# Performance work log

Hardware: AMD Instinct MI355X
Metric: run time of the kernel (lower is better)

## Reference

```python
import jax, jax.numpy as jnp
import numpy as np

S, B, K, H = 2048, 256, 64, 128  # seq_len, batch, process_dim, hidden_size


def softplus10(x):
    return jax.nn.softplus(10.0 * x) / 10.0


def setup_inputs() -> dict:
    key = jax.random.key(0)
    ks = jax.random.split(key, 10)
    sc = 0.1
    dt = jax.random.uniform(ks[0], (S, B), dtype=jnp.float32)
    seq_types = jax.random.randint(ks[1], (S, B), 0, K)  # in [0, K); K is padding idx
    h0 = jnp.zeros((B, H), dtype=jnp.float32)
    embed_W = jax.random.normal(ks[2], (K + 1, K), dtype=jnp.float32) * sc
    embed_W = embed_W.at[K].set(0.0)  # padding_idx row is zero
    W_ih = jax.random.normal(ks[3], (H, K), dtype=jnp.float32) * sc
    b_ih = jax.random.normal(ks[4], (H,), dtype=jnp.float32) * sc
    W_hh = jax.random.normal(ks[5], (H, H), dtype=jnp.float32) * sc
    b_hh = jax.random.normal(ks[6], (H,), dtype=jnp.float32) * sc
    dec_W = jax.random.normal(ks[7], (H, K + H), dtype=jnp.float32) * sc
    dec_b = jax.random.normal(ks[8], (H,), dtype=jnp.float32) * sc
    return {"dt": dt, "h0": h0, "embed_W": embed_W, "W_ih": W_ih, "b_ih": b_ih,
            "W_hh": W_hh, "b_hh": b_hh, "dec_W": dec_W, "dec_b": dec_b,
            "seq_types": seq_types}


def reference(dt, h0, embed_W, W_ih, b_ih, W_hh, b_hh, dec_W, dec_b, seq_types):
    # Per-event recurrence: h(t) = hidden_i * exp(-decay_i * dt_i)
    def step(h, inp):
        dt_t, ty_t = inp                     # [B], [B]
        x = embed_W[ty_t]                    # [B, K] embedding lookup
        concat = jnp.concatenate([x, h], axis=1)          # [B, K+H]
        decay = softplus10(concat @ dec_W.T + dec_b)      # [B, H]
        hidden = jnp.tanh(x @ W_ih.T + b_ih + h @ W_hh.T + b_hh)  # RNNCell tanh
        h_new = hidden * jnp.exp(-decay * dt_t[:, None])  # decayed hidden state
        return h_new, (hidden, decay, h_new)

    _, (hiddens, decays, hiddens_ti) = jax.lax.scan(step, h0, (dt, seq_types))
    # each: [S, B, H], matching the per-step lists of the torch module
    return hiddens, decays, hiddens_ti
```

## Files before the change

kernel.cpp:

```cpp
#include <hip/hip_runtime.h>

#define SEQ 2048
#define BAT 256
#define KD  64
#define HD  128
#define SBH 67108864u

typedef _Float16 half2v  __attribute__((ext_vector_type(2)));
typedef __fp16   fp16x2  __attribute__((ext_vector_type(2)));
typedef unsigned uint2v  __attribute__((ext_vector_type(2)));

template<int CTRL>
__device__ __forceinline__ float dpp_add(float keep, float send) {
    const int r = __builtin_amdgcn_update_dpp(0, __float_as_int(send),
                                              CTRL, 0xF, 0xF, true);
    return keep + __int_as_float(r);
}

__device__ __forceinline__ float xchg32(float v, int hi_half, int lane) {
#if __has_builtin(__builtin_amdgcn_permlane32_swap)
    uint2v r = __builtin_amdgcn_permlane32_swap(__float_as_uint(v),
                                                __float_as_uint(v),
                                                false, false);
    return __uint_as_float(hi_half ? r.x : r.y);
#else
    return __uint_as_float(__builtin_amdgcn_ds_bpermute(
        ((lane ^ 32) << 2), __float_as_uint(v)));
#endif
}

__device__ __forceinline__ int PK(float a, float b) {
    fp16x2 p = __builtin_amdgcn_cvt_pkrtz(a, b);
    return __builtin_bit_cast(int, p);
}

__device__ __forceinline__ float fdot2(int w, int h, float c) {
#if __has_builtin(__builtin_amdgcn_fdot2)
    return __builtin_amdgcn_fdot2(__builtin_bit_cast(half2v, w),
                                  __builtin_bit_cast(half2v, h), c, false);
#else
    half2v wv = __builtin_bit_cast(half2v, w), hv = __builtin_bit_cast(half2v, h);
    return fmaf((float)wv[1], (float)hv[1], fmaf((float)wv[0], (float)hv[0], c));
#endif
}

#define PIN(x) asm volatile("" : "+v"(x))
#define PIN4(v4) PIN(v4.x); PIN(v4.y); PIN(v4.z); PIN(v4.w)

#define STEP_BARRIER() do {                                   \
    asm volatile("s_waitcnt lgkmcnt(0)" ::: "memory");        \
    __builtin_amdgcn_s_barrier();                             \
    asm volatile("" ::: "memory");                            \
} while (0)

__global__ __launch_bounds__(128) void precompute_tables(
    const float* __restrict__ embed_W, const float* __restrict__ W_ih,
    const float* __restrict__ b_ih,    const float* __restrict__ b_hh,
    const float* __restrict__ dec_W,   const float* __restrict__ dec_b,
    float* __restrict__ tabH, float* __restrict__ tabD)
{
    __shared__ float x[KD];
    const int ty = blockIdx.x;
    const int r  = threadIdx.x;
    if (r < KD) x[r] = embed_W[ty * KD + r];
    __syncthreads();
    float ah = 0.f, ad = 0.f;
#pragma unroll
    for (int k = 0; k < KD; ++k) {
        const float xv = x[k];
        ah += xv * W_ih[r * KD + k];
        ad += xv * dec_W[r * (KD + HD) + k];
    }
    tabH[ty * HD + r] = ah + b_ih[r] + b_hh[r];
    tabD[ty * HD + r] = ad + dec_b[r];
}

__global__ __launch_bounds__(256, 1) void hawkes_rnn(
    const float* __restrict__ dt_g,  const float* __restrict__ h0,
    const float* __restrict__ W_hh,  const float* __restrict__ dec_W,
    const int*   __restrict__ seq_types,
    const float* __restrict__ tabH,  const float* __restrict__ tabD,
    float* __restrict__ out)
{
    __shared__ __align__(16) _Float16 h16[2][HD];
    __shared__ __align__(8) int2 dtty[SEQ + 2];
    __shared__ _Float16 tabLH[(KD + 1) * HD];
    __shared__ _Float16 tabLD[(KD + 1) * HD];

    const int b    = blockIdx.x;
    const int tid  = threadIdx.x;
    const int lane = tid & 63;
    const int b0 = lane & 1, b1 = (lane >> 1) & 1;
    const int b2 = (lane >> 2) & 1, b3 = (lane >> 3) & 1;
    const int b4 = (lane >> 4) & 1, b5 = (lane >> 5) & 1;
    const int G     = (tid >> 6) * 4 + b4 * 2 + b2;
    const int row   = 8 * G + 4 * b0 + 2 * b1 + b3;
    const int chunk = b0 | (b1 << 1) | (b3 << 2);

    for (int t = tid; t < SEQ; t += 256) {
        dtty[t] = make_int2(__float_as_int(dt_g[(size_t)t * BAT + b]),
                            seq_types[(size_t)t * BAT + b]);
    }
    if (tid < 2) dtty[SEQ + tid] = make_int2(0, 0);
    for (int i = tid; i < (KD + 1) * HD; i += 256) {
        tabLH[i] = (_Float16)tabH[i];
        tabLD[i] = (_Float16)tabD[i];
    }
    if (tid < HD) h16[0][tid] = (_Float16)h0[b * HD + tid];

    const size_t rstr = b5 ? (size_t)(KD + HD) : (size_t)HD;
    const float* wb = (b5 ? (dec_W + KD) : W_hh) + (size_t)(8 * G) * rstr
                      + chunk * 16;
#define LWROW(DA, DB, P) { \
    const float4 _a = *reinterpret_cast<const float4*>(P);        \
    const float4 _b = *reinterpret_cast<const float4*>((P) + 4);  \
    const float4 _c = *reinterpret_cast<const float4*>((P) + 8);  \
    const float4 _d = *reinterpret_cast<const float4*>((P) + 12); \
    DA = make_int4(PK(_a.x,_a.y), PK(_a.z,_a.w), PK(_b.x,_b.y), PK(_b.z,_b.w)); \
    DB = make_int4(PK(_c.x,_c.y), PK(_c.z,_c.w), PK(_d.x,_d.y), PK(_d.z,_d.w)); }
    int4 w0a,w0b,w1a,w1b,w2a,w2b,w3a,w3b,w4a,w4b,w5a,w5b,w6a,w6b,w7a,w7b;
    LWROW(w0a,w0b, wb + 0 * rstr)  LWROW(w1a,w1b, wb + 1 * rstr)
    LWROW(w2a,w2b, wb + 2 * rstr)  LWROW(w3a,w3b, wb + 3 * rstr)
    LWROW(w4a,w4b, wb + 4 * rstr)  LWROW(w5a,w5b, wb + 5 * rstr)
    LWROW(w6a,w6b, wb + 6 * rstr)  LWROW(w7a,w7b, wb + 7 * rstr)
#undef LWROW
    PIN4(w0a); PIN4(w0b); PIN4(w1a); PIN4(w1b);
    PIN4(w2a); PIN4(w2b); PIN4(w3a); PIN4(w3b);
    PIN4(w4a); PIN4(w4b); PIN4(w5a); PIN4(w5b);
    PIN4(w6a); PIN4(w6b); PIN4(w7a); PIN4(w7b);

    const _Float16* tabp = (b5 ? tabLD : tabLH) + row;

    unsigned off = (unsigned)(b * HD + row);

    __syncthreads();

    int2 pr_cur = dtty[0];
    int2 pr_nxt = dtty[1];
    float tab_cur = (float)tabp[pr_cur.y * HD];
    float tab_nxt = (float)tabp[pr_nxt.y * HD];

#define DOT16(A, WA, WB) \
    A = fdot2(WA.x, hv0.x, A); A = fdot2(WA.y, hv0.y, A); \
    A = fdot2(WA.z, hv0.z, A); A = fdot2(WA.w, hv0.w, A); \
    A = fdot2(WB.x, hv1.x, A); A = fdot2(WB.y, hv1.y, A); \
    A = fdot2(WB.z, hv1.z, A); A = fdot2(WB.w, hv1.w, A);

#define STEP(P, TT) { \
    const int2 pr_pf = dtty[(TT) + 2];                \
    const float tab_pf = (float)tabp[pr_pf.y * HD];   \
    const float dtv = __int_as_float(pr_cur.x); \
     \
    const int4 hv0 = *reinterpret_cast<const int4*>(&h16[P][chunk * 16]); \
    const int4 hv1 = *reinterpret_cast<const int4*>(&h16[P][chunk * 16 + 8]); \
    float a0 = 0.f, a1 = 0.f, a2 = 0.f, a3 = 0.f; \
    float a4 = 0.f, a5 = 0.f, a6 = 0.f, a7 = 0.f; \
    DOT16(a0, w0a, w0b)  DOT16(a1, w1a, w1b) \
    DOT16(a2, w2a, w2b)  DOT16(a3, w3a, w3b) \
    DOT16(a4, w4a, w4b)  DOT16(a5, w5a, w5b) \
    DOT16(a6, w6a, w6b)  DOT16(a7, w7a, w7b) \
     \
    const float t0 = dpp_add<0xB1>(b0 ? a4 : a0, b0 ? a0 : a4); \
    const float t1 = dpp_add<0xB1>(b0 ? a5 : a1, b0 ? a1 : a5); \
    const float t2 = dpp_add<0xB1>(b0 ? a6 : a2, b0 ? a2 : a6); \
    const float t3 = dpp_add<0xB1>(b0 ? a7 : a3, b0 ? a3 : a7); \
     \
    const float u0 = dpp_add<0x4E>(b1 ? t2 : t0, b1 ? t0 : t2); \
    const float u1 = dpp_add<0x4E>(b1 ? t3 : t1, b1 ? t1 : t3); \
     \
    const float sv = dpp_add<0x128>(b3 ? u1 : u0, b3 ? u0 : u1) + tab_cur; \
     \
    const float e2 = __expf(2.f * sv); \
    const float vh = 1.f - __fdividef(2.f, e2 + 1.f);             \
    const float z  = 10.f * sv; \
    const float em = __expf(-fabsf(z)); \
    const float sp = 0.1f * (fmaxf(z, 0.f) + __logf(1.f + em));   \
    const float vd = __expf(-sp * dtv); \
    const float v  = b5 ? vd : vh; \
     \
    const float cross = xchg32(v, b5, lane); \
    const float hnew  = v * cross; \
    if (b5 == 0) { \
        h16[(P) ^ 1][row] = (_Float16)hnew;    \
        out[off] = v; \
        out[off + 2u * SBH] = hnew; \
    } else { \
        out[off + SBH] = sp; \
    } \
    off += BAT * HD; \
    pr_cur = pr_nxt;   pr_nxt = pr_pf; \
    tab_cur = tab_nxt; tab_nxt = tab_pf; \
    STEP_BARRIER(); \
}

    for (int t = 0; t < SEQ; t += 2) {
        STEP(0, t)
        STEP(1, t + 1)
    }
#undef STEP
#undef DOT16
}

extern "C" void kernel_launch(void* const* d_in, const int* in_sizes, int n_in,
                              void* d_out, int out_size, void* d_ws, size_t ws_size,
                              hipStream_t stream) {
    const float* dt        = (const float*)d_in[0];
    const float* h0        = (const float*)d_in[1];
    const float* embed_W   = (const float*)d_in[2];
    const float* W_ih      = (const float*)d_in[3];
    const float* b_ih      = (const float*)d_in[4];
    const float* W_hh      = (const float*)d_in[5];
    const float* b_hh      = (const float*)d_in[6];
    const float* dec_W     = (const float*)d_in[7];
    const float* dec_b     = (const float*)d_in[8];
    const int*   seq_types = (const int*)  d_in[9];
    float* out  = (float*)d_out;

    float* tabHw = (float*)d_ws;
    float* tabDw = tabHw + (KD + 1) * HD;

    precompute_tables<<<KD + 1, 128, 0, stream>>>(embed_W, W_ih, b_ih, b_hh,
                                                  dec_W, dec_b, tabHw, tabDw);
    hawkes_rnn<<<BAT, 256, 0, stream>>>(dt, h0, W_hh, dec_W, seq_types,
                                        tabHw, tabDw, out);
}
```

Baseline: 824.4 us.

## Map one thread per hidden row computing both hidden and decay dot products

Reworks the recurrent kernel from 256 threads, where each lane computes a partial 16-element dot product for 8 rows, to 128 threads, where each thread owns one hidden row and computes both full 128-length dot products (W_hh and the dec_W hidden part). This removes the DPP reduction tree and the permlane32 cross-half exchange, and each thread now writes all three outputs. In exchange, each thread holds twice as many packed-fp16 weight registers (128 VGPRs of weights), reads the whole h vector from LDS each step, and runs a longer serial dot-product chain per step.

```diff
diff --git a/kernel.cpp b/kernel.cpp
--- a/kernel.cpp
+++ b/kernel.cpp
@@ -8,26 +8,6 @@
 
 typedef _Float16 half2v  __attribute__((ext_vector_type(2)));
 typedef __fp16   fp16x2  __attribute__((ext_vector_type(2)));
-typedef unsigned uint2v  __attribute__((ext_vector_type(2)));
-
-template<int CTRL>
-__device__ __forceinline__ float dpp_add(float keep, float send) {
-    const int r = __builtin_amdgcn_update_dpp(0, __float_as_int(send),
-                                              CTRL, 0xF, 0xF, true);
-    return keep + __int_as_float(r);
-}
-
-__device__ __forceinline__ float xchg32(float v, int hi_half, int lane) {
-#if __has_builtin(__builtin_amdgcn_permlane32_swap)
-    uint2v r = __builtin_amdgcn_permlane32_swap(__float_as_uint(v),
-                                                __float_as_uint(v),
-                                                false, false);
-    return __uint_as_float(hi_half ? r.x : r.y);
-#else
-    return __uint_as_float(__builtin_amdgcn_ds_bpermute(
-        ((lane ^ 32) << 2), __float_as_uint(v)));
-#endif
-}
 
 __device__ __forceinline__ int PK(float a, float b) {
     fp16x2 p = __builtin_amdgcn_cvt_pkrtz(a, b);
@@ -75,7 +55,7 @@
     tabD[ty * HD + r] = ad + dec_b[r];
 }
 
-__global__ __launch_bounds__(256, 1) void hawkes_rnn(
+__global__ __launch_bounds__(128, 1) void hawkes_rnn(
     const float* __restrict__ dt_g,  const float* __restrict__ h0,
     const float* __restrict__ W_hh,  const float* __restrict__ dec_W,
     const int*   __restrict__ seq_types,
@@ -87,49 +67,46 @@
     __shared__ _Float16 tabLH[(KD + 1) * HD];
     __shared__ _Float16 tabLD[(KD + 1) * HD];
 
-    const int b    = blockIdx.x;
-    const int tid  = threadIdx.x;
-    const int lane = tid & 63;
-    const int b0 = lane & 1, b1 = (lane >> 1) & 1;
-    const int b2 = (lane >> 2) & 1, b3 = (lane >> 3) & 1;
-    const int b4 = (lane >> 4) & 1, b5 = (lane >> 5) & 1;
-    const int G     = (tid >> 6) * 4 + b4 * 2 + b2;
-    const int row   = 8 * G + 4 * b0 + 2 * b1 + b3;
-    const int chunk = b0 | (b1 << 1) | (b3 << 2);
-
-    for (int t = tid; t < SEQ; t += 256) {
+    const int b   = blockIdx.x;
+    const int tid = threadIdx.x;
+    const int row = tid;
+
+    for (int t = tid; t < SEQ; t += 128) {
         dtty[t] = make_int2(__float_as_int(dt_g[(size_t)t * BAT + b]),
                             seq_types[(size_t)t * BAT + b]);
     }
     if (tid < 2) dtty[SEQ + tid] = make_int2(0, 0);
-    for (int i = tid; i < (KD + 1) * HD; i += 256) {
+    for (int i = tid; i < (KD + 1) * HD; i += 128) {
         tabLH[i] = (_Float16)tabH[i];
         tabLD[i] = (_Float16)tabD[i];
     }
-    if (tid < HD) h16[0][tid] = (_Float16)h0[b * HD + tid];
-
-    const size_t rstr = b5 ? (size_t)(KD + HD) : (size_t)HD;
-    const float* wb = (b5 ? (dec_W + KD) : W_hh) + (size_t)(8 * G) * rstr
-                      + chunk * 16;
-#define LWROW(DA, DB, P) { \
-    const float4 _a = *reinterpret_cast<const float4*>(P);        \
-    const float4 _b = *reinterpret_cast<const float4*>((P) + 4);  \
-    const float4 _c = *reinterpret_cast<const float4*>((P) + 8);  \
-    const float4 _d = *reinterpret_cast<const float4*>((P) + 12); \
-    DA = make_int4(PK(_a.x,_a.y), PK(_a.z,_a.w), PK(_b.x,_b.y), PK(_b.z,_b.w)); \
-    DB = make_int4(PK(_c.x,_c.y), PK(_c.z,_c.w), PK(_d.x,_d.y), PK(_d.z,_d.w)); }
-    int4 w0a,w0b,w1a,w1b,w2a,w2b,w3a,w3b,w4a,w4b,w5a,w5b,w6a,w6b,w7a,w7b;
-    LWROW(w0a,w0b, wb + 0 * rstr)  LWROW(w1a,w1b, wb + 1 * rstr)
-    LWROW(w2a,w2b, wb + 2 * rstr)  LWROW(w3a,w3b, wb + 3 * rstr)
-    LWROW(w4a,w4b, wb + 4 * rstr)  LWROW(w5a,w5b, wb + 5 * rstr)
-    LWROW(w6a,w6b, wb + 6 * rstr)  LWROW(w7a,w7b, wb + 7 * rstr)
-#undef LWROW
-    PIN4(w0a); PIN4(w0b); PIN4(w1a); PIN4(w1b);
-    PIN4(w2a); PIN4(w2b); PIN4(w3a); PIN4(w3b);
-    PIN4(w4a); PIN4(w4b); PIN4(w5a); PIN4(w5b);
-    PIN4(w6a); PIN4(w6b); PIN4(w7a); PIN4(w7b);
-
-    const _Float16* tabp = (b5 ? tabLD : tabLH) + row;
+    h16[0][tid] = (_Float16)h0[b * HD + tid];
+
+    const float* wh = W_hh  + (size_t)row * HD;
+    const float* wd = dec_W + (size_t)row * (KD + HD) + KD;
+#define LQ(D, P) { \
+    const float4 _a = *reinterpret_cast<const float4*>(P);       \
+    const float4 _b = *reinterpret_cast<const float4*>((P) + 4); \
+    D = make_int4(PK(_a.x,_a.y), PK(_a.z,_a.w), PK(_b.x,_b.y), PK(_b.z,_b.w)); }
+    int4 wh0,wh1,wh2,wh3,wh4,wh5,wh6,wh7,wh8,wh9,wh10,wh11,wh12,wh13,wh14,wh15;
+    int4 wd0,wd1,wd2,wd3,wd4,wd5,wd6,wd7,wd8,wd9,wd10,wd11,wd12,wd13,wd14,wd15;
+    LQ(wh0,  wh +   0) LQ(wh1,  wh +   8) LQ(wh2,  wh +  16) LQ(wh3,  wh +  24)
+    LQ(wh4,  wh +  32) LQ(wh5,  wh +  40) LQ(wh6,  wh +  48) LQ(wh7,  wh +  56)
+    LQ(wh8,  wh +  64) LQ(wh9,  wh +  72) LQ(wh10, wh +  80) LQ(wh11, wh +  88)
+    LQ(wh12, wh +  96) LQ(wh13, wh + 104) LQ(wh14, wh + 112) LQ(wh15, wh + 120)
+    LQ(wd0,  wd +   0) LQ(wd1,  wd +   8) LQ(wd2,  wd +  16) LQ(wd3,  wd +  24)
+    LQ(wd4,  wd +  32) LQ(wd5,  wd +  40) LQ(wd6,  wd +  48) LQ(wd7,  wd +  56)
+    LQ(wd8,  wd +  64) LQ(wd9,  wd +  72) LQ(wd10, wd +  80) LQ(wd11, wd +  88)
+    LQ(wd12, wd +  96) LQ(wd13, wd + 104) LQ(wd14, wd + 112) LQ(wd15, wd + 120)
+#undef LQ
+    PIN4(wh0); PIN4(wh1); PIN4(wh2); PIN4(wh3);
+    PIN4(wh4); PIN4(wh5); PIN4(wh6); PIN4(wh7);
+    PIN4(wh8); PIN4(wh9); PIN4(wh10);PIN4(wh11);
+    PIN4(wh12);PIN4(wh13);PIN4(wh14);PIN4(wh15);
+    PIN4(wd0); PIN4(wd1); PIN4(wd2); PIN4(wd3);
+    PIN4(wd4); PIN4(wd5); PIN4(wd6); PIN4(wd7);
+    PIN4(wd8); PIN4(wd9); PIN4(wd10);PIN4(wd11);
+    PIN4(wd12);PIN4(wd13);PIN4(wd14);PIN4(wd15);
 
     unsigned off = (unsigned)(b * HD + row);
 
@@ -137,59 +114,64 @@
 
     int2 pr_cur = dtty[0];
     int2 pr_nxt = dtty[1];
-    float tab_cur = (float)tabp[pr_cur.y * HD];
-    float tab_nxt = (float)tabp[pr_nxt.y * HD];
-
-#define DOT16(A, WA, WB) \
-    A = fdot2(WA.x, hv0.x, A); A = fdot2(WA.y, hv0.y, A); \
-    A = fdot2(WA.z, hv0.z, A); A = fdot2(WA.w, hv0.w, A); \
-    A = fdot2(WB.x, hv1.x, A); A = fdot2(WB.y, hv1.y, A); \
-    A = fdot2(WB.z, hv1.z, A); A = fdot2(WB.w, hv1.w, A);
+    float tabH_cur = (float)tabLH[pr_cur.y * HD + row];
+    float tabD_cur = (float)tabLD[pr_cur.y * HD + row];
+    float tabH_nxt = (float)tabLH[pr_nxt.y * HD + row];
+    float tabD_nxt = (float)tabLD[pr_nxt.y * HD + row];
+
+#define HBATCH(I0, WH_A, WH_B, WH_C, WH_D, WD_A, WD_B, WD_C, WD_D, AH, AD) { \
+    const int4 hA = hsrc[(I0) + 0]; \
+    const int4 hB = hsrc[(I0) + 1]; \
+    const int4 hC = hsrc[(I0) + 2]; \
+    const int4 hD = hsrc[(I0) + 3]; \
+    AH = fdot2(WH_A.x, hA.x, AH); AH = fdot2(WH_A.y, hA.y, AH); \
+    AH = fdot2(WH_A.z, hA.z, AH); AH = fdot2(WH_A.w, hA.w, AH); \
+    AD = fdot2(WD_A.x, hA.x, AD); AD = fdot2(WD_A.y, hA.y, AD); \
+    AD = fdot2(WD_A.z, hA.z, AD); AD = fdot2(WD_A.w, hA.w, AD); \
+    AH = fdot2(WH_B.x, hB.x, AH); AH = fdot2(WH_B.y, hB.y, AH); \
+    AH = fdot2(WH_B.z, hB.z, AH); AH = fdot2(WH_B.w, hB.w, AH); \
+    AD = fdot2(WD_B.x, hB.x, AD); AD = fdot2(WD_B.y, hB.y, AD); \
+    AD = fdot2(WD_B.z, hB.z, AD); AD = fdot2(WD_B.w, hB.w, AD); \
+    AH = fdot2(WH_C.x, hC.x, AH); AH = fdot2(WH_C.y, hC.y, AH); \
+    AH = fdot2(WH_C.z, hC.z, AH); AH = fdot2(WH_C.w, hC.w, AH); \
+    AD = fdot2(WD_C.x, hC.x, AD); AD = fdot2(WD_C.y, hC.y, AD); \
+    AD = fdot2(WD_C.z, hC.z, AD); AD = fdot2(WD_C.w, hC.w, AD); \
+    AH = fdot2(WH_D.x, hD.x, AH); AH = fdot2(WH_D.y, hD.y, AH); \
+    AH = fdot2(WH_D.z, hD.z, AH); AH = fdot2(WH_D.w, hD.w, AH); \
+    AD = fdot2(WD_D.x, hD.x, AD); AD = fdot2(WD_D.y, hD.y, AD); \
+    AD = fdot2(WD_D.z, hD.z, AD); AD = fdot2(WD_D.w, hD.w, AD); \
+}
 
 #define STEP(P, TT) { \
-    const int2 pr_pf = dtty[(TT) + 2];                \
-    const float tab_pf = (float)tabp[pr_pf.y * HD];   \
+    const int2 pr_pf = dtty[(TT) + 2]; \
+    const float tabH_pf = (float)tabLH[pr_pf.y * HD + row]; \
+    const float tabD_pf = (float)tabLD[pr_pf.y * HD + row]; \
     const float dtv = __int_as_float(pr_cur.x); \
+    const int4* hsrc = reinterpret_cast<const int4*>(&h16[P][0]); \
+    float aH0 = 0.f, aH1 = 0.f, aH2 = 0.f, aH3 = 0.f; \
+    float aD0 = 0.f, aD1 = 0.f, aD2 = 0.f, aD3 = 0.f; \
+    HBATCH(0,  wh0, wh1, wh2, wh3,  wd0, wd1, wd2, wd3,  aH0, aD0) \
+    HBATCH(4,  wh4, wh5, wh6, wh7,  wd4, wd5, wd6, wd7,  aH1, aD1) \
+    HBATCH(8,  wh8, wh9, wh10,wh11, wd8, wd9, wd10,wd11, aH2, aD2) \
+    HBATCH(12, wh12,wh13,wh14,wh15, wd12,wd13,wd14,wd15, aH3, aD3) \
+    const float svH = (aH0 + aH1) + (aH2 + aH3) + tabH_cur; \
+    const float svD = (aD0 + aD1) + (aD2 + aD3) + tabD_cur; \
      \
-    const int4 hv0 = *reinterpret_cast<const int4*>(&h16[P][chunk * 16]); \
-    const int4 hv1 = *reinterpret_cast<const int4*>(&h16[P][chunk * 16 + 8]); \
-    float a0 = 0.f, a1 = 0.f, a2 = 0.f, a3 = 0.f; \
-    float a4 = 0.f, a5 = 0.f, a6 = 0.f, a7 = 0.f; \
-    DOT16(a0, w0a, w0b)  DOT16(a1, w1a, w1b) \
-    DOT16(a2, w2a, w2b)  DOT16(a3, w3a, w3b) \
-    DOT16(a4, w4a, w4b)  DOT16(a5, w5a, w5b) \
-    DOT16(a6, w6a, w6b)  DOT16(a7, w7a, w7b) \
-     \
-    const float t0 = dpp_add<0xB1>(b0 ? a4 : a0, b0 ? a0 : a4); \
-    const float t1 = dpp_add<0xB1>(b0 ? a5 : a1, b0 ? a1 : a5); \
-    const float t2 = dpp_add<0xB1>(b0 ? a6 : a2, b0 ? a2 : a6); \
-    const float t3 = dpp_add<0xB1>(b0 ? a7 : a3, b0 ? a3 : a7); \
-     \
-    const float u0 = dpp_add<0x4E>(b1 ? t2 : t0, b1 ? t0 : t2); \
-    const float u1 = dpp_add<0x4E>(b1 ? t3 : t1, b1 ? t1 : t3); \
-     \
-    const float sv = dpp_add<0x128>(b3 ? u1 : u0, b3 ? u0 : u1) + tab_cur; \
-     \
-    const float e2 = __expf(2.f * sv); \
+    const float e2 = __expf(2.f * svH); \
     const float vh = 1.f - __fdividef(2.f, e2 + 1.f);             \
-    const float z  = 10.f * sv; \
+    const float z  = 10.f * svD; \
     const float em = __expf(-fabsf(z)); \
     const float sp = 0.1f * (fmaxf(z, 0.f) + __logf(1.f + em));   \
     const float vd = __expf(-sp * dtv); \
-    const float v  = b5 ? vd : vh; \
-     \
-    const float cross = xchg32(v, b5, lane); \
-    const float hnew  = v * cross; \
-    if (b5 == 0) { \
-        h16[(P) ^ 1][row] = (_Float16)hnew;    \
-        out[off] = v; \
-        out[off + 2u * SBH] = hnew; \
-    } else { \
-        out[off + SBH] = sp; \
-    } \
+    const float hnew = vh * vd;           \
+    h16[(P) ^ 1][row] = (_Float16)hnew;   \
+    out[off] = vh; \
+    out[off + SBH] = sp; \
+    out[off + 2u * SBH] = hnew; \
     off += BAT * HD; \
-    pr_cur = pr_nxt;   pr_nxt = pr_pf; \
-    tab_cur = tab_nxt; tab_nxt = tab_pf; \
+    pr_cur = pr_nxt;     pr_nxt = pr_pf; \
+    tabH_cur = tabH_nxt; tabH_nxt = tabH_pf; \
+    tabD_cur = tabD_nxt; tabD_nxt = tabD_pf; \
     STEP_BARRIER(); \
 }
 
@@ -198,7 +180,7 @@
         STEP(1, t + 1)
     }
 #undef STEP
-#undef DOT16
+#undef HBATCH
 }
 
 extern "C" void kernel_launch(void* const* d_in, const int* in_sizes, int n_in,
@@ -221,6 +203,6 @@
 
     precompute_tables<<<KD + 1, 128, 0, stream>>>(embed_W, W_ih, b_ih, b_hh,
                                                   dec_W, dec_b, tabHw, tabDw);
-    hawkes_rnn<<<BAT, 256, 0, stream>>>(dt, h0, W_hh, dec_W, seq_types,
+    hawkes_rnn<<<BAT, 128, 0, stream>>>(dt, h0, W_hh, dec_W, seq_types,
                                         tabHw, tabDw, out);
 }
```

After: 1.035 ms. 25.5% more time.

## Defer global stores past barrier and pre-permute weight rows to drop DPP selects

Applied to the files above, without the earlier changes.

Each step's output stores are postponed to the start of the next step and issued after the shared h16 load, so they leave the critical path between the state update and the barrier. The eight weight rows each lane loads are permuted with r0 XOR index, so the DPP butterfly reduction no longer needs per-lane select instructions before each add. This adds a peeled first step, a trailing store after the loop, and two extra live registers.

```diff
diff --git a/kernel.cpp b/kernel.cpp
--- a/kernel.cpp
+++ b/kernel.cpp
@@ -94,7 +94,8 @@
     const int b2 = (lane >> 2) & 1, b3 = (lane >> 3) & 1;
     const int b4 = (lane >> 4) & 1, b5 = (lane >> 5) & 1;
     const int G     = (tid >> 6) * 4 + b4 * 2 + b2;
-    const int row   = 8 * G + 4 * b0 + 2 * b1 + b3;
+    const int r0_   = 4 * b0 + 2 * b1 + b3;
+    const int row   = 8 * G + r0_;
     const int chunk = b0 | (b1 << 1) | (b3 << 2);
 
     for (int t = tid; t < SEQ; t += 256) {
@@ -109,20 +110,20 @@
     if (tid < HD) h16[0][tid] = (_Float16)h0[b * HD + tid];
 
     const size_t rstr = b5 ? (size_t)(KD + HD) : (size_t)HD;
-    const float* wb = (b5 ? (dec_W + KD) : W_hh) + (size_t)(8 * G) * rstr
-                      + chunk * 16;
-#define LWROW(DA, DB, P) { \
-    const float4 _a = *reinterpret_cast<const float4*>(P);        \
-    const float4 _b = *reinterpret_cast<const float4*>((P) + 4);  \
-    const float4 _c = *reinterpret_cast<const float4*>((P) + 8);  \
-    const float4 _d = *reinterpret_cast<const float4*>((P) + 12); \
+    const float* mat = (b5 ? (dec_W + KD) : W_hh);
+#define LWROW(DA, DB, S) { \
+    const float* _p = mat + (size_t)(8 * G + (r0_ ^ (S))) * rstr + chunk * 16; \
+    const float4 _a = *reinterpret_cast<const float4*>(_p);        \
+    const float4 _b = *reinterpret_cast<const float4*>(_p + 4);    \
+    const float4 _c = *reinterpret_cast<const float4*>(_p + 8);    \
+    const float4 _d = *reinterpret_cast<const float4*>(_p + 12);   \
     DA = make_int4(PK(_a.x,_a.y), PK(_a.z,_a.w), PK(_b.x,_b.y), PK(_b.z,_b.w)); \
     DB = make_int4(PK(_c.x,_c.y), PK(_c.z,_c.w), PK(_d.x,_d.y), PK(_d.z,_d.w)); }
     int4 w0a,w0b,w1a,w1b,w2a,w2b,w3a,w3b,w4a,w4b,w5a,w5b,w6a,w6b,w7a,w7b;
-    LWROW(w0a,w0b, wb + 0 * rstr)  LWROW(w1a,w1b, wb + 1 * rstr)
-    LWROW(w2a,w2b, wb + 2 * rstr)  LWROW(w3a,w3b, wb + 3 * rstr)
-    LWROW(w4a,w4b, wb + 4 * rstr)  LWROW(w5a,w5b, wb + 5 * rstr)
-    LWROW(w6a,w6b, wb + 6 * rstr)  LWROW(w7a,w7b, wb + 7 * rstr)
+    LWROW(w0a,w0b, 0)  LWROW(w1a,w1b, 1)
+    LWROW(w2a,w2b, 2)  LWROW(w3a,w3b, 3)
+    LWROW(w4a,w4b, 4)  LWROW(w5a,w5b, 5)
+    LWROW(w6a,w6b, 6)  LWROW(w7a,w7b, 7)
 #undef LWROW
     PIN4(w0a); PIN4(w0b); PIN4(w1a); PIN4(w1b);
     PIN4(w2a); PIN4(w2b); PIN4(w3a); PIN4(w3b);
@@ -140,19 +141,26 @@
     float tab_cur = (float)tabp[pr_cur.y * HD];
     float tab_nxt = (float)tabp[pr_nxt.y * HD];
 
+    float stv_c = 0.f, hnew_c = 0.f;
+
 #define DOT16(A, WA, WB) \
     A = fdot2(WA.x, hv0.x, A); A = fdot2(WA.y, hv0.y, A); \
     A = fdot2(WA.z, hv0.z, A); A = fdot2(WA.w, hv0.w, A); \
     A = fdot2(WB.x, hv1.x, A); A = fdot2(WB.y, hv1.y, A); \
     A = fdot2(WB.z, hv1.z, A); A = fdot2(WB.w, hv1.w, A);
 
-#define STEP(P, TT) { \
+#define STEP(P, TT, DOST) { \
+     \
+    const int4 hv0 = *reinterpret_cast<const int4*>(&h16[P][chunk * 16]); \
+    const int4 hv1 = *reinterpret_cast<const int4*>(&h16[P][chunk * 16 + 8]); \
+    if (DOST) {                          \
+        if (b5 == 0) { out[off] = stv_c; out[off + 2u * SBH] = hnew_c; } \
+        else         { out[off + SBH] = stv_c; } \
+        off += BAT * HD; \
+    } \
     const int2 pr_pf = dtty[(TT) + 2];                \
     const float tab_pf = (float)tabp[pr_pf.y * HD];   \
     const float dtv = __int_as_float(pr_cur.x); \
-     \
-    const int4 hv0 = *reinterpret_cast<const int4*>(&h16[P][chunk * 16]); \
-    const int4 hv1 = *reinterpret_cast<const int4*>(&h16[P][chunk * 16 + 8]); \
     float a0 = 0.f, a1 = 0.f, a2 = 0.f, a3 = 0.f; \
     float a4 = 0.f, a5 = 0.f, a6 = 0.f, a7 = 0.f; \
     DOT16(a0, w0a, w0b)  DOT16(a1, w1a, w1b) \
@@ -160,15 +168,14 @@
     DOT16(a4, w4a, w4b)  DOT16(a5, w5a, w5b) \
     DOT16(a6, w6a, w6b)  DOT16(a7, w7a, w7b) \
      \
-    const float t0 = dpp_add<0xB1>(b0 ? a4 : a0, b0 ? a0 : a4); \
-    const float t1 = dpp_add<0xB1>(b0 ? a5 : a1, b0 ? a1 : a5); \
-    const float t2 = dpp_add<0xB1>(b0 ? a6 : a2, b0 ? a2 : a6); \
-    const float t3 = dpp_add<0xB1>(b0 ? a7 : a3, b0 ? a3 : a7); \
-     \
-    const float u0 = dpp_add<0x4E>(b1 ? t2 : t0, b1 ? t0 : t2); \
-    const float u1 = dpp_add<0x4E>(b1 ? t3 : t1, b1 ? t1 : t3); \
-     \
-    const float sv = dpp_add<0x128>(b3 ? u1 : u0, b3 ? u0 : u1) + tab_cur; \
+     \
+    const float t0 = dpp_add<0xB1>(a0, a4); \
+    const float t1 = dpp_add<0xB1>(a1, a5); \
+    const float t2 = dpp_add<0xB1>(a2, a6); \
+    const float t3 = dpp_add<0xB1>(a3, a7); \
+    const float u0 = dpp_add<0x4E>(t0, t2); \
+    const float u1 = dpp_add<0x4E>(t1, t3); \
+    const float sv = dpp_add<0x128>(u0, u1) + tab_cur; \
      \
     const float e2 = __expf(2.f * sv); \
     const float vh = 1.f - __fdividef(2.f, e2 + 1.f);             \
@@ -180,23 +187,22 @@
      \
     const float cross = xchg32(v, b5, lane); \
     const float hnew  = v * cross; \
-    if (b5 == 0) { \
-        h16[(P) ^ 1][row] = (_Float16)hnew;    \
-        out[off] = v; \
-        out[off + 2u * SBH] = hnew; \
-    } else { \
-        out[off + SBH] = sp; \
-    } \
-    off += BAT * HD; \
+    if (b5 == 0) h16[(P) ^ 1][row] = (_Float16)hnew;    \
+    stv_c  = b5 ? sp : v; \
+    hnew_c = hnew; \
     pr_cur = pr_nxt;   pr_nxt = pr_pf; \
     tab_cur = tab_nxt; tab_nxt = tab_pf; \
     STEP_BARRIER(); \
 }
 
-    for (int t = 0; t < SEQ; t += 2) {
-        STEP(0, t)
-        STEP(1, t + 1)
-    }
+    STEP(0, 0, 0)
+    STEP(1, 1, 1)
+    for (int t = 2; t < SEQ; t += 2) {
+        STEP(0, t, 1)
+        STEP(1, t + 1, 1)
+    }
+    if (b5 == 0) { out[off] = stv_c; out[off + 2u * SBH] = hnew_c; }
+    else         { out[off + SBH] = stv_c; }
 #undef STEP
 #undef DOT16
 }
```

New measurement: 798.9 us (median of 2 runs). 1.03x faster.
